# Kernel optimization log

Measured on AMD Instinct MI355X. Metric: run time of the kernel, lower is better.

The kernel has to match this reference:

```python
import jax, jax.numpy as jnp
import numpy as np

B, CIN, COUT, H, W = 32, 256, 512, 32, 32
ITERS = 20


def setup_inputs() -> dict:
    key = jax.random.key(0)
    k1, k2 = jax.random.split(key)
    inp = jax.random.uniform(k1, (B, CIN, H, W), dtype=jnp.float32)
    # weight ~ U(init_min=0, init_max=1), shape [out_channels, in_channels] (1x1 kernel squeezed)
    weight = jax.random.uniform(k2, (COUT, CIN), dtype=jnp.float32)
    return {"input": inp, "weight": weight}


def reference(input, weight):
    # Linear (use_convolution=False) path of NNMFConv2dP with 1x1 kernel.
    x = jnp.moveaxis(input, 1, -1)                      # [B, H, W, Cin]
    c_out = weight.shape[0]
    h0 = jnp.full(x.shape[:3] + (c_out,), 1.0 / c_out, dtype=x.dtype)  # [B, H, W, Cout]

    def body(_, h):
        # reconstruction = F.linear(h, weight.T) = h @ weight  -> [B, H, W, Cin]
        rec = h @ weight + 1e-20
        # h *= F.linear(x / rec, weight) = (x / rec) @ weight.T -> [B, H, W, Cout]
        h = h * ((x / rec) @ weight.T)
        # channel normalization
        return h / (h.sum(-1, keepdims=True) + 1e-19)

    h = jax.lax.fori_loop(0, ITERS, body, h0)
    return jnp.moveaxis(h, -1, 1)                       # [B, Cout, H, W]
```

## Files before the change

### kernel.cpp

```cpp
#include <hip/hip_runtime.h>

#define CIN   256
#define COUT  512
#define HW    1024
#define ITERS 20

typedef __attribute__((ext_vector_type(8)))  short bf16x8;
typedef __attribute__((ext_vector_type(4)))  float f32x4;
typedef __attribute__((ext_vector_type(16))) float f32x16;
typedef __attribute__((ext_vector_type(2)))  unsigned u32x2;

__device__ __forceinline__ unsigned short f2b(float x) {
  unsigned b = __builtin_bit_cast(unsigned, x);
  unsigned r = (b + 0x7FFFu + ((b >> 16) & 1u)) >> 16;
  return (unsigned short)r;
}
__device__ __forceinline__ unsigned cvt_pk_bf16(float a, float b) {
  unsigned r;
  asm("v_cvt_pk_bf16_f32 %0, %1, %2" : "=v"(r) : "v"(a), "v"(b));
  return r;
}

__global__ __launch_bounds__(256) void prep_weights(const float* __restrict__ w,
                                                    unsigned short* __restrict__ w1,
                                                    unsigned short* __restrict__ w2) {
  int f = blockIdx.x * 256 + threadIdx.x;
  {
    int i = f & 7, l = (f >> 3) & 63, kt = (f >> 9) & 31, ct = f >> 14;
    int c = ct * 32 + (l & 31);
    int j = kt * 16 + ((l >> 5) << 3) + i;
    w1[f] = f2b(w[j * CIN + c]);
  }
  {
    int i = f & 7, l = (f >> 3) & 63, kt = (f >> 9) & 15, jt = f >> 13;
    int j = jt * 32 + (l & 31);
    int c = kt * 16 + ((l >> 5) << 3) + i;
    w2[f] = f2b(w[j * CIN + c]);
  }
}

__global__ __launch_bounds__(1024, 4) void nnmf_kernel(const float* __restrict__ xin,
                                                       const unsigned short* __restrict__ w1,
                                                       const unsigned short* __restrict__ w2,
                                                       float* __restrict__ out) {
  __shared__ __align__(16) unsigned short hA[2 * 32 * 512];
  __shared__ __align__(16) unsigned short yF[2 * 16 * 512];
  __shared__ __align__(16) unsigned xS[2 * 8 * 4 * 2 * 32 * 2];
  __shared__ float red[2 * 32 * 20];

  const int tid  = threadIdx.x;
  const int wv   = tid >> 6;
  const int lane = tid & 63;
  const int px   = lane & 31;
  const int hi   = lane >> 5;

  const int ct = wv >> 1;
  const int pA = wv & 1;
  const int jt = wv;

  const int wg     = blockIdx.x;
  const int bb     = wg >> 4;
  const int hwbase = (wg & 15) * 64;
  const float* xbase = xin + (size_t)bb * (CIN * HW) + hwbase + px;

#pragma unroll
  for (int rb = 0; rb < 4; ++rb) {
    int c0 = ct * 32 + 8 * rb + 4 * hi;
    const float* xp = xbase + pA * 32;
    u32x2 pk = { cvt_pk_bf16(xp[c0 * HW],       xp[(c0 + 1) * HW]),
                 cvt_pk_bf16(xp[(c0 + 2) * HW], xp[(c0 + 3) * HW]) };
    *(u32x2*)(xS + (((((pA * 8 + ct) * 4 + rb) * 2 + hi) * 32 + px) << 1)) = pk;
  }

  {
    unsigned* h32 = (unsigned*)hA;
#pragma unroll
    for (int g = 0; g < 16; ++g) h32[tid + (g << 10)] = 0x3B003B00u;
  }

  f32x16 hreg[2];
#pragma unroll
  for (int pt = 0; pt < 2; ++pt)
#pragma unroll
    for (int r = 0; r < 16; ++r) hreg[pt][r] = 1.0f / 512.0f;

  const unsigned short* w1w = w1 + (size_t)ct * (32 * 512) + lane * 8;
  const unsigned short* w2w = w2 + (size_t)jt * (16 * 512) + lane * 8;
  const unsigned short* hAp = hA + pA * (32 * 512) + lane * 8;
  const unsigned short* yFr = yF + lane * 8;

  __syncthreads();

  for (int it = 0; it < ITERS; ++it) {
    f32x16 acc1;
#pragma unroll
    for (int r = 0; r < 16; ++r) acc1[r] = 0.0f;

#pragma unroll 4
    for (int kt = 0; kt < 32; ++kt) {
      bf16x8 a = *(const bf16x8*)(w1w + kt * 512);
      bf16x8 b = *(const bf16x8*)(hAp + kt * 512);
      acc1 = __builtin_amdgcn_mfma_f32_32x32x16_bf16(a, b, acc1, 0, 0, 0);
    }

#pragma unroll
    for (int rb = 0; rb < 4; ++rb) {
      u32x2 xp = *(const u32x2*)(xS + (((((pA * 8 + ct) * 4 + rb) * 2 + hi) * 32 + px) << 1));
      float x0 = __builtin_bit_cast(float, xp.x << 16);
      float x1 = __builtin_bit_cast(float, xp.x & 0xffff0000u);
      float x2 = __builtin_bit_cast(float, xp.y << 16);
      float x3 = __builtin_bit_cast(float, xp.y & 0xffff0000u);
      float y0 = x0 * __builtin_amdgcn_rcpf(acc1[4 * rb + 0] + 1e-20f);
      float y1 = x1 * __builtin_amdgcn_rcpf(acc1[4 * rb + 1] + 1e-20f);
      float y2 = x2 * __builtin_amdgcn_rcpf(acc1[4 * rb + 2] + 1e-20f);
      float y3 = x3 * __builtin_amdgcn_rcpf(acc1[4 * rb + 3] + 1e-20f);
      int kt2 = ct * 2 + (rb >> 1);
      u32x2 pk = { cvt_pk_bf16(y0, y1), cvt_pk_bf16(y2, y3) };
      *(u32x2*)(yF + (((pA * 16 + kt2) * 64 + ((rb & 1) << 5) + px) << 3) + (hi << 2)) = pk;
    }
    __syncthreads();

    f32x16 acc2[2];
#pragma unroll
    for (int pt = 0; pt < 2; ++pt)
#pragma unroll
      for (int r = 0; r < 16; ++r) acc2[pt][r] = 0.0f;

#pragma unroll 2
    for (int kt = 0; kt < 16; ++kt) {
      bf16x8 a  = *(const bf16x8*)(w2w + kt * 512);
      bf16x8 b0 = *(const bf16x8*)(yFr + kt * 512);
      bf16x8 b1 = *(const bf16x8*)(yFr + (16 + kt) * 512);
      acc2[0] = __builtin_amdgcn_mfma_f32_32x32x16_bf16(a, b0, acc2[0], 0, 0, 0);
      acc2[1] = __builtin_amdgcn_mfma_f32_32x32x16_bf16(a, b1, acc2[1], 0, 0, 0);
    }

    float psum0 = 0.0f, psum1 = 0.0f;
#pragma unroll
    for (int r = 0; r < 16; ++r) {
      float hn0 = hreg[0][r] * acc2[0][r];
      float hn1 = hreg[1][r] * acc2[1][r];
      hreg[0][r] = hn0;
      hreg[1][r] = hn1;
      psum0 += hn0;
      psum1 += hn1;
    }
    psum0 += __shfl_xor(psum0, 32, 64);
    psum1 += __shfl_xor(psum1, 32, 64);
    if (lane < 32) {
      red[(0 * 32 + px) * 20 + wv] = psum0;
      red[(1 * 32 + px) * 20 + wv] = psum1;
    }
    __syncthreads();

    float inv[2];
#pragma unroll
    for (int pt = 0; pt < 2; ++pt) {
      const float* rp = red + (pt * 32 + px) * 20;
      f32x4 s0 = *(const f32x4*)(rp + 0);
      f32x4 s1 = *(const f32x4*)(rp + 4);
      f32x4 s2 = *(const f32x4*)(rp + 8);
      f32x4 s3 = *(const f32x4*)(rp + 12);
      float s = (s0[0]+s0[1]+s0[2]+s0[3]) + (s1[0]+s1[1]+s1[2]+s1[3])
              + (s2[0]+s2[1]+s2[2]+s2[3]) + (s3[0]+s3[1]+s3[2]+s3[3]);
      inv[pt] = __builtin_amdgcn_rcpf(s + 1e-19f);
    }

    if (it < ITERS - 1) {
#pragma unroll
      for (int pt = 0; pt < 2; ++pt)
#pragma unroll
        for (int rb = 0; rb < 4; ++rb) {
          float h0 = hreg[pt][4 * rb + 0] * inv[pt];
          float h1 = hreg[pt][4 * rb + 1] * inv[pt];
          float h2 = hreg[pt][4 * rb + 2] * inv[pt];
          float h3 = hreg[pt][4 * rb + 3] * inv[pt];
          hreg[pt][4 * rb + 0] = h0; hreg[pt][4 * rb + 1] = h1;
          hreg[pt][4 * rb + 2] = h2; hreg[pt][4 * rb + 3] = h3;
          int kt = wv * 2 + (rb >> 1);
          u32x2 pk = { cvt_pk_bf16(h0, h1), cvt_pk_bf16(h2, h3) };
          *(u32x2*)(hA + (((pt * 32 + kt) * 64 + ((rb & 1) << 5) + px) << 3) + (hi << 2)) = pk;
        }
    } else {
      float* obase = out + (size_t)bb * (COUT * HW) + hwbase + px;
#pragma unroll
      for (int pt = 0; pt < 2; ++pt)
#pragma unroll
        for (int r = 0; r < 16; ++r) {
          int j = wv * 32 + (r & 3) + 8 * (r >> 2) + 4 * hi;
          obase[j * HW + pt * 32] = hreg[pt][r] * inv[pt];
        }
    }
    __syncthreads();
  }
}

extern "C" void kernel_launch(void* const* d_in, const int* in_sizes, int n_in,
                              void* d_out, int out_size, void* d_ws, size_t ws_size,
                              hipStream_t stream) {
  const float* x = (const float*)d_in[0];
  const float* w = (const float*)d_in[1];
  unsigned short* w1 = (unsigned short*)d_ws;
  unsigned short* w2 = w1 + COUT * CIN;
  float* out = (float*)d_out;

  prep_weights<<<dim3(512), dim3(256), 0, stream>>>(w, w1, w2);
  nnmf_kernel<<<dim3(512), dim3(1024), 0, stream>>>(x, w1, w2, out);
}
```

Baseline: 490.1 us.

## Defer channel normalization into next iteration to drop a barrier, split GEMM1 accumulators

New measurement: 451.3 us. 1.09x faster.

```diff
diff --git a/kernel.cpp b/kernel.cpp
--- a/kernel.cpp
+++ b/kernel.cpp
@@ -84,6 +84,8 @@
 #pragma unroll
     for (int r = 0; r < 16; ++r) hreg[pt][r] = 1.0f / 512.0f;
 
+  float invv0 = 1.0f, invv1 = 1.0f;
+
   const unsigned short* w1w = w1 + (size_t)ct * (32 * 512) + lane * 8;
   const unsigned short* w2w = w2 + (size_t)jt * (16 * 512) + lane * 8;
   const unsigned short* hAp = hA + pA * (32 * 512) + lane * 8;
@@ -92,31 +94,41 @@
   __syncthreads();
 
   for (int it = 0; it < ITERS; ++it) {
-    f32x16 acc1;
-#pragma unroll
-    for (int r = 0; r < 16; ++r) acc1[r] = 0.0f;
-
-#pragma unroll 4
-    for (int kt = 0; kt < 32; ++kt) {
-      bf16x8 a = *(const bf16x8*)(w1w + kt * 512);
-      bf16x8 b = *(const bf16x8*)(hAp + kt * 512);
-      acc1 = __builtin_amdgcn_mfma_f32_32x32x16_bf16(a, b, acc1, 0, 0, 0);
-    }
-
-#pragma unroll
-    for (int rb = 0; rb < 4; ++rb) {
-      u32x2 xp = *(const u32x2*)(xS + (((((pA * 8 + ct) * 4 + rb) * 2 + hi) * 32 + px) << 1));
-      float x0 = __builtin_bit_cast(float, xp.x << 16);
-      float x1 = __builtin_bit_cast(float, xp.x & 0xffff0000u);
-      float x2 = __builtin_bit_cast(float, xp.y << 16);
-      float x3 = __builtin_bit_cast(float, xp.y & 0xffff0000u);
-      float y0 = x0 * __builtin_amdgcn_rcpf(acc1[4 * rb + 0] + 1e-20f);
-      float y1 = x1 * __builtin_amdgcn_rcpf(acc1[4 * rb + 1] + 1e-20f);
-      float y2 = x2 * __builtin_amdgcn_rcpf(acc1[4 * rb + 2] + 1e-20f);
-      float y3 = x3 * __builtin_amdgcn_rcpf(acc1[4 * rb + 3] + 1e-20f);
-      int kt2 = ct * 2 + (rb >> 1);
-      u32x2 pk = { cvt_pk_bf16(y0, y1), cvt_pk_bf16(y2, y3) };
-      *(u32x2*)(yF + (((pA * 16 + kt2) * 64 + ((rb & 1) << 5) + px) << 3) + (hi << 2)) = pk;
+    f32x16 acc1a, acc1b;
+#pragma unroll
+    for (int r = 0; r < 16; ++r) { acc1a[r] = 0.0f; acc1b[r] = 0.0f; }
+
+#pragma unroll 2
+    for (int kt = 0; kt < 16; ++kt) {
+      bf16x8 a0 = *(const bf16x8*)(w1w + kt * 512);
+      bf16x8 b0 = *(const bf16x8*)(hAp + kt * 512);
+      bf16x8 a1 = *(const bf16x8*)(w1w + (16 + kt) * 512);
+      bf16x8 b1 = *(const bf16x8*)(hAp + (16 + kt) * 512);
+      acc1a = __builtin_amdgcn_mfma_f32_32x32x16_bf16(a0, b0, acc1a, 0, 0, 0);
+      acc1b = __builtin_amdgcn_mfma_f32_32x32x16_bf16(a1, b1, acc1b, 0, 0, 0);
+    }
+
+    {
+      float ainv = pA ? invv1 : invv0;
+#pragma unroll
+      for (int rb = 0; rb < 4; ++rb) {
+        u32x2 xp = *(const u32x2*)(xS + (((((pA * 8 + ct) * 4 + rb) * 2 + hi) * 32 + px) << 1));
+        float x0 = __builtin_bit_cast(float, xp.x << 16);
+        float x1 = __builtin_bit_cast(float, xp.x & 0xffff0000u);
+        float x2 = __builtin_bit_cast(float, xp.y << 16);
+        float x3 = __builtin_bit_cast(float, xp.y & 0xffff0000u);
+        float r0 = acc1a[4 * rb + 0] + acc1b[4 * rb + 0];
+        float r1 = acc1a[4 * rb + 1] + acc1b[4 * rb + 1];
+        float r2 = acc1a[4 * rb + 2] + acc1b[4 * rb + 2];
+        float r3 = acc1a[4 * rb + 3] + acc1b[4 * rb + 3];
+        float y0 = x0 * __builtin_amdgcn_rcpf(ainv * r0 + 1e-20f);
+        float y1 = x1 * __builtin_amdgcn_rcpf(ainv * r1 + 1e-20f);
+        float y2 = x2 * __builtin_amdgcn_rcpf(ainv * r2 + 1e-20f);
+        float y3 = x3 * __builtin_amdgcn_rcpf(ainv * r3 + 1e-20f);
+        int kt2 = ct * 2 + (rb >> 1);
+        u32x2 pk = { cvt_pk_bf16(y0, y1), cvt_pk_bf16(y2, y3) };
+        *(u32x2*)(yF + (((pA * 16 + kt2) * 64 + ((rb & 1) << 5) + px) << 3) + (hi << 2)) = pk;
+      }
     }
     __syncthreads();
 
@@ -138,8 +150,8 @@
     float psum0 = 0.0f, psum1 = 0.0f;
 #pragma unroll
     for (int r = 0; r < 16; ++r) {
-      float hn0 = hreg[0][r] * acc2[0][r];
-      float hn1 = hreg[1][r] * acc2[1][r];
+      float hn0 = hreg[0][r] * invv0 * acc2[0][r];
+      float hn1 = hreg[1][r] * invv1 * acc2[1][r];
       hreg[0][r] = hn0;
       hreg[1][r] = hn1;
       psum0 += hn0;
@@ -151,47 +163,54 @@
       red[(0 * 32 + px) * 20 + wv] = psum0;
       red[(1 * 32 + px) * 20 + wv] = psum1;
     }
-    __syncthreads();
-
-    float inv[2];
-#pragma unroll
-    for (int pt = 0; pt < 2; ++pt) {
-      const float* rp = red + (pt * 32 + px) * 20;
-      f32x4 s0 = *(const f32x4*)(rp + 0);
-      f32x4 s1 = *(const f32x4*)(rp + 4);
-      f32x4 s2 = *(const f32x4*)(rp + 8);
-      f32x4 s3 = *(const f32x4*)(rp + 12);
-      float s = (s0[0]+s0[1]+s0[2]+s0[3]) + (s1[0]+s1[1]+s1[2]+s1[3])
-              + (s2[0]+s2[1]+s2[2]+s2[3]) + (s3[0]+s3[1]+s3[2]+s3[3]);
-      inv[pt] = __builtin_amdgcn_rcpf(s + 1e-19f);
-    }
 
     if (it < ITERS - 1) {
 #pragma unroll
       for (int pt = 0; pt < 2; ++pt)
 #pragma unroll
         for (int rb = 0; rb < 4; ++rb) {
-          float h0 = hreg[pt][4 * rb + 0] * inv[pt];
-          float h1 = hreg[pt][4 * rb + 1] * inv[pt];
-          float h2 = hreg[pt][4 * rb + 2] * inv[pt];
-          float h3 = hreg[pt][4 * rb + 3] * inv[pt];
-          hreg[pt][4 * rb + 0] = h0; hreg[pt][4 * rb + 1] = h1;
-          hreg[pt][4 * rb + 2] = h2; hreg[pt][4 * rb + 3] = h3;
+          float h0 = hreg[pt][4 * rb + 0];
+          float h1 = hreg[pt][4 * rb + 1];
+          float h2 = hreg[pt][4 * rb + 2];
+          float h3 = hreg[pt][4 * rb + 3];
           int kt = wv * 2 + (rb >> 1);
           u32x2 pk = { cvt_pk_bf16(h0, h1), cvt_pk_bf16(h2, h3) };
           *(u32x2*)(hA + (((pt * 32 + kt) * 64 + ((rb & 1) << 5) + px) << 3) + (hi << 2)) = pk;
         }
-    } else {
-      float* obase = out + (size_t)bb * (COUT * HW) + hwbase + px;
-#pragma unroll
-      for (int pt = 0; pt < 2; ++pt)
-#pragma unroll
-        for (int r = 0; r < 16; ++r) {
-          int j = wv * 32 + (r & 3) + 8 * (r >> 2) + 4 * hi;
-          obase[j * HW + pt * 32] = hreg[pt][r] * inv[pt];
-        }
     }
     __syncthreads();
+
+    {
+      const float* rp0 = red + (0 * 32 + px) * 20;
+      f32x4 a0 = *(const f32x4*)(rp0 + 0);
+      f32x4 a1 = *(const f32x4*)(rp0 + 4);
+      f32x4 a2 = *(const f32x4*)(rp0 + 8);
+      f32x4 a3 = *(const f32x4*)(rp0 + 12);
+      float s0 = (a0[0]+a0[1]+a0[2]+a0[3]) + (a1[0]+a1[1]+a1[2]+a1[3])
+               + (a2[0]+a2[1]+a2[2]+a2[3]) + (a3[0]+a3[1]+a3[2]+a3[3]);
+      invv0 = __builtin_amdgcn_rcpf(s0 + 1e-19f);
+      const float* rp1 = red + (1 * 32 + px) * 20;
+      f32x4 b0 = *(const f32x4*)(rp1 + 0);
+      f32x4 b1 = *(const f32x4*)(rp1 + 4);
+      f32x4 b2 = *(const f32x4*)(rp1 + 8);
+      f32x4 b3 = *(const f32x4*)(rp1 + 12);
+      float s1 = (b0[0]+b0[1]+b0[2]+b0[3]) + (b1[0]+b1[1]+b1[2]+b1[3])
+               + (b2[0]+b2[1]+b2[2]+b2[3]) + (b3[0]+b3[1]+b3[2]+b3[3]);
+      invv1 = __builtin_amdgcn_rcpf(s1 + 1e-19f);
+    }
+  }
+
+  {
+    float* obase = out + (size_t)bb * (COUT * HW) + hwbase + px;
+#pragma unroll
+    for (int pt = 0; pt < 2; ++pt) {
+      float fin = pt ? invv1 : invv0;
+#pragma unroll
+      for (int r = 0; r < 16; ++r) {
+        int j = wv * 32 + (r & 3) + 8 * (r >> 2) + 4 * hi;
+        obase[j * HW + pt * 32] = hreg[pt][r] * fin;
+      }
+    }
   }
 }
 
```
